# Kernel optimization log

Measured on AMD Instinct MI355X. Metric: run time of the kernel, lower is better.

Reference implementation:

```python
import jax, jax.numpy as jnp
import numpy as np

N_FACTORS = 8
T_BINS = 512
N_NEURONS = 512
N_TRIALS = 128
JITTER = 1e-3


def setup_inputs() -> dict:
    key = jax.random.key(0)
    k1, k2, k3, k4, k5 = jax.random.split(key, 5)
    return {
        "spike_data": jax.random.normal(k1, (N_TRIALS, N_NEURONS, T_BINS), dtype=jnp.float32),
        "Cm": jax.random.normal(k2, (N_NEURONS, N_FACTORS), dtype=jnp.float32),
        "dm": jax.random.normal(k3, (N_NEURONS,), dtype=jnp.float32),
        "r_diag": jax.random.uniform(k4, (N_NEURONS,), dtype=jnp.float32),
        "gamma_m": jax.random.uniform(k5, (N_FACTORS,), dtype=jnp.float32),
    }


def reference(spike_data, Cm, dm, r_diag, gamma_m):
    """GPFA e-step posterior mean.

    Faithful to Multi_populations_GPFA: per-factor SE-kernel GP covariances
    (make_K_big), block-striped inverse (make_K_big_inv), precision
    M = K_big_inv + blockdiag(C' R^-1 C), minv = inv(M) (inv_persymm returns
    exactly inv(M) for persymmetric M), x_mean = minv @ vec(C' R^-1 (y - d)).
    Row ordering is index = t * n_factors + f, matching K_big[i::F, i::F].
    """
    F = N_FACTORS
    n_trials, n_neurons, T = spike_data.shape
    dtype = spike_data.dtype

    # Per-factor GP covariances: K_f = (1-jitter)*exp(-gamma_f/2 * Tdif^2) + jitter*I
    t = jnp.arange(T, dtype=dtype)
    Tdif2 = (t[:, None] - t[None, :]) ** 2                      # (T, T)
    K = (1.0 - JITTER) * jnp.exp(-0.5 * gamma_m[:, None, None] * Tdif2) \
        + JITTER * jnp.eye(T, dtype=dtype)                       # (F, T, T)
    K_inv = jnp.linalg.inv(K)                                    # batched per factor

    # rinv = diag(1/diag(Rm));  c_rinv = C' R^-1;  c_rinv_c = C' R^-1 C
    rinv = 1.0 / r_diag                                          # (N,)
    c_rinv = Cm.T * rinv[None, :]                                # (F, N)
    c_rinv_c = c_rinv @ Cm                                       # (F, F)

    # M[t,i,u,j] = K_inv[i,t,u]*delta_ij + c_rinv_c[i,j]*delta_tu
    eyeF = jnp.eye(F, dtype=dtype)
    eyeT = jnp.eye(T, dtype=dtype)
    M = (jnp.einsum('ftu,ij->tiuj', K_inv, eyeF)
         + jnp.einsum('tu,ij->tiuj', eyeT, c_rinv_c)).reshape(F * T, F * T)
    minv = jnp.linalg.inv(M)                                     # (F*T, F*T)

    # term1[t*F+f, trial] = (C' R^-1 (y - d))[f, trial, t]
    dif = spike_data - dm[None, :, None]                         # (trials, N, T)
    term1 = jnp.einsum('fn,rnt->tfr', c_rinv, dif).reshape(F * T, n_trials)

    x_mean = (minv @ term1).reshape(T, F, n_trials)              # (T, F, trials)
    return jnp.transpose(x_mean, (2, 1, 0))                      # (trials, F, T)
```

## Files before the change

### kernel.cpp

```cpp
#include <hip/hip_runtime.h>


#define NF 8
#define TBINS 512
#define NNEU 512
#define NTRI 128
#define PAD 68

#define OFF_A0     0
#define OFF_A1     2097152
#define OFF_CRVT   4194304
#define OFF_CRVVT  4198400
#define OFF_CCT    4202496
#define OFF_CD     4202560
#define OFF_CDV    4202624
#define OFF_RINV   4202688
#define OFF_LAM    4203200
#define OFF_VF     4203216
#define OFF_BT     4203280
#define OFF_XT     4727568
#define OFF_PP0    5251856
#define OFF_PP1    5284624

__device__ __forceinline__ void load8(float* v, const float* ptr){
  float4 a = ((const float4*)ptr)[0];
  float4 b = ((const float4*)ptr)[1];
  v[0]=a.x; v[1]=a.y; v[2]=a.z; v[3]=a.w;
  v[4]=b.x; v[5]=b.y; v[6]=b.z; v[7]=b.w;
}
__device__ __forceinline__ void store8(float* ptr, const float* v){
  ((float4*)ptr)[0] = make_float4(v[0],v[1],v[2],v[3]);
  ((float4*)ptr)[1] = make_float4(v[4],v[5],v[6],v[7]);
}

__device__ __forceinline__ float rlane(float v, int l){
  return __int_as_float(__builtin_amdgcn_readlane(__float_as_int(v), l));
}

template<int KK>
__device__ __forceinline__ void gj_reg_step(float (&c)[64], int lane){
  float pivot = rlane(c[KK], KK);
  float pinv  = 1.0f / pivot;
  float newr  = c[KK] * pinv;
  bool iskk = (lane == KK);
  #pragma unroll
  for (int i = 0; i < KK; ++i){
    float pc = rlane(c[i], KK);
    c[i] = iskk ? (-pc * pinv) : (c[i] - pc * newr);
  }
  #pragma unroll
  for (int i = KK + 1; i < 64; ++i){
    float pc = rlane(c[i], KK);
    c[i] = iskk ? (-pc * pinv) : (c[i] - pc * newr);
  }
  c[KK] = iskk ? pinv : newr;
}

template<int KK> struct GJChain {
  static __device__ __forceinline__ void run(float (&c)[64], int lane){
    gj_reg_step<KK>(c, lane);
    GJChain<KK + 1>::run(c, lane);
  }
};
template<> struct GJChain<64> {
  static __device__ __forceinline__ void run(float (&c)[64], int lane){}
};

__global__ void prep_kernel(const float* __restrict__ Cm, const float* __restrict__ dm,
                            const float* __restrict__ r_diag,
                            float* __restrict__ crvT, float* __restrict__ ccT,
                            float* __restrict__ cd, float* __restrict__ rinv){
  __shared__ float s_crv[NNEU*NF];
  __shared__ float s_cm[NNEU*NF];
  __shared__ float s_dm[NNEU];
  int tid = threadIdx.x;
  float ri = 1.0f / r_diag[tid];
  rinv[tid] = ri;
  s_dm[tid] = dm[tid];
  #pragma unroll
  for (int f = 0; f < NF; ++f){
    float cv = Cm[tid*NF + f];
    s_cm[tid*NF + f] = cv;
    float v = cv * ri;
    s_crv[tid*NF + f] = v;
    crvT[tid*NF + f] = v;
  }
  __syncthreads();
  if (tid < 64){
    int f = tid >> 3, g = tid & 7;
    float acc = 0.f;
    for (int n = 0; n < NNEU; ++n) acc += s_crv[n*NF+f] * s_cm[n*NF+g];
    ccT[tid] = acc;
  } else if (tid < 72){
    int f = tid - 64;
    float acc = 0.f;
    for (int n = 0; n < NNEU; ++n) acc += s_crv[n*NF+f] * s_dm[n];
    cd[f] = acc;
  }
}

__global__ void eig8_kernel(const float* __restrict__ ccT,
                            float* __restrict__ Vf, float* __restrict__ lam){
  int lane = threadIdx.x & 63;
  int a = lane >> 3, b = lane & 7;
  float Av = ccT[lane];
  float Vv = (a == b) ? 1.0f : 0.0f;
  for (int sw = 0; sw < 8; ++sw){
    for (int p = 0; p < 7; ++p){
      for (int q = p + 1; q < 8; ++q){
        float apq = __shfl(Av, p*8 + q, 64);
        if (fabsf(apq) < 1e-20f) continue;
        float app = __shfl(Av, p*8 + p, 64);
        float aqq = __shfl(Av, q*8 + q, 64);
        float beta = (aqq - app) / (2.0f * apq);
        float tt = ((beta >= 0.0f) ? 1.0f : -1.0f) / (fabsf(beta) + sqrtf(1.0f + beta*beta));
        float c = 1.0f / sqrtf(1.0f + tt*tt);
        float s = tt * c;
        int bp = (b == p) ? q : (b == q) ? p : b;
        float Ac = __shfl(Av, a*8 + bp, 64);
        float Vc = __shfl(Vv, a*8 + bp, 64);
        if (b == p)      { Av = c*Av - s*Ac;  Vv = c*Vv - s*Vc; }
        else if (b == q) { Av = s*Ac + c*Av;  Vv = s*Vc + c*Vv; }
        int ap = (a == p) ? q : (a == q) ? p : a;
        float Ar = __shfl(Av, ap*8 + b, 64);
        if (a == p)      Av = c*Av - s*Ar;
        else if (a == q) Av = s*Ar + c*Av;
      }
    }
  }
  if (a == b) lam[a] = Av;
  Vf[lane] = Vv;
}

__global__ void rotv_kernel(const float* __restrict__ crvT, const float* __restrict__ cd,
                            const float* __restrict__ Vf,
                            float* __restrict__ crvVT, float* __restrict__ cdV){
  __shared__ float Vl[64];
  int tid = threadIdx.x;
  if (tid < 64) Vl[tid] = Vf[tid];
  __syncthreads();
  float cv[8], ov[8];
  load8(cv, crvT + tid*8);
  #pragma unroll
  for (int i = 0; i < 8; ++i){
    float s = 0.f;
    #pragma unroll
    for (int f = 0; f < 8; ++f) s += Vl[f*8+i] * cv[f];
    ov[i] = s;
  }
  store8(crvVT + tid*8, ov);
  if (tid < 8){
    float s = 0.f;
    #pragma unroll
    for (int f = 0; f < 8; ++f) s += Vl[f*8+tid] * cd[f];
    cdV[tid] = s;
  }
}

__global__ void buildK_kernel(const float* __restrict__ gamma, float* __restrict__ A0){
  int f = blockIdx.y;
  int idx = blockIdx.x*256 + threadIdx.x;
  int t = idx >> 9, u = idx & 511;
  float g = gamma[f];
  float d = (float)(t - u);
  float v = 0.999f * expf(-0.5f * g * d * d);
  if (t == u) v += 1.0e-3f;
  A0[(size_t)f*TBINS*TBINS + idx] = v;
}

__global__ void buildG_kernel(const float* __restrict__ A0, const float* __restrict__ lam,
                              float* __restrict__ A1){
  int idx = blockIdx.x*256 + threadIdx.x;
  float s = 0.f;
  #pragma unroll
  for (int f2 = 0; f2 < NF; ++f2) s += A0[(size_t)f2*TBINS*TBINS + idx];
  bool diag = ((idx >> 9) == (idx & 511));
  #pragma unroll
  for (int i = 0; i < NF; ++i)
    A1[(size_t)i*TBINS*TBINS + idx] = s + (diag ? lam[i] : 0.f);
}

__global__ __launch_bounds__(64) void gj_pivot0(const float* __restrict__ A,
                                                float* __restrict__ Pout){
  int f = blockIdx.x;
  int lane = threadIdx.x;
  const float* Af = A + (size_t)f*TBINS*TBINS;
  float c[64];
  #pragma unroll
  for (int i = 0; i < 64; ++i) c[i] = Af[(size_t)i*TBINS + lane];
  GJChain<0>::run(c, lane);
  #pragma unroll
  for (int i = 0; i < 64; ++i) Pout[f*4096 + i*64 + lane] = c[i];
}

#define ACC4(tm, fm) \
  tm[0] += fm.x*s0.x + fm.y*s1.x + fm.z*s2.x + fm.w*s3.x; \
  tm[1] += fm.x*s0.y + fm.y*s1.y + fm.z*s2.y + fm.w*s3.y; \
  tm[2] += fm.x*s0.z + fm.y*s1.z + fm.z*s2.z + fm.w*s3.z; \
  tm[3] += fm.x*s0.w + fm.y*s1.w + fm.z*s2.w + fm.w*s3.w;

__global__ __launch_bounds__(256) void gj_apply(const float* __restrict__ src,
                                                float* __restrict__ dst,
                                                const float* __restrict__ Pin,
                                                float* __restrict__ Pout,
                                                int k, int inv_next){
  __shared__ float P[64*PAD];
  __shared__ float Q[64*PAD];
  __shared__ float F[64*PAD];
  int f  = blockIdx.y;
  int ti = blockIdx.x >> 3, tj = blockIdx.x & 7;
  int tid = threadIdx.x;
  const float* A = src + (size_t)f*TBINS*TBINS;
  float* D = dst + (size_t)f*TBINS*TBINS;

  for (int v = tid; v < 1024; v += 256){
    int r = v >> 4, c4 = (v & 15) << 2;
    *(float4*)&P[r*PAD + c4] = *(const float4*)(Pin + f*4096 + r*64 + c4);
  }
  if (tj != k){
    for (int v = tid; v < 1024; v += 256){
      int r = v >> 4, c4 = (v & 15) << 2;
      *(float4*)&Q[r*PAD + c4] = *(const float4*)(A + (size_t)(k*64+r)*TBINS + tj*64 + c4);
    }
  }
  if (ti != k){
    for (int v = tid; v < 1024; v += 256){
      int r = v >> 4, c4 = (v & 15) << 2;
      *(float4*)&F[r*PAD + c4] = *(const float4*)(A + (size_t)(ti*64+r)*TBINS + k*64 + c4);
    }
  }
  __syncthreads();

  int jg = (tid & 15) << 2;
  int ib = (tid >> 4) << 2;

  if (tj == k){
    if (ti == k){
      for (int v = tid; v < 1024; v += 256){
        int r = v >> 4, c4 = (v & 15) << 2;
        *(float4*)(D + (size_t)(k*64+r)*TBINS + k*64 + c4) = *(float4*)&P[r*PAD + c4];
      }
      return;
    }
    float w[4][4] = {{0.f,0.f,0.f,0.f},{0.f,0.f,0.f,0.f},{0.f,0.f,0.f,0.f},{0.f,0.f,0.f,0.f}};
    for (int u4 = 0; u4 < 64; u4 += 4){
      float4 f0 = *(float4*)&F[(ib+0)*PAD + u4];
      float4 f1 = *(float4*)&F[(ib+1)*PAD + u4];
      float4 f2 = *(float4*)&F[(ib+2)*PAD + u4];
      float4 f3 = *(float4*)&F[(ib+3)*PAD + u4];
      float4 s0 = *(float4*)&P[(u4+0)*PAD + jg];
      float4 s1 = *(float4*)&P[(u4+1)*PAD + jg];
      float4 s2 = *(float4*)&P[(u4+2)*PAD + jg];
      float4 s3 = *(float4*)&P[(u4+3)*PAD + jg];
      ACC4(w[0], f0); ACC4(w[1], f1); ACC4(w[2], f2); ACC4(w[3], f3);
    }
    #pragma unroll
    for (int m = 0; m < 4; ++m)
      *(float4*)(D + (size_t)(ti*64+ib+m)*TBINS + k*64 + jg)
        = make_float4(-w[m][0], -w[m][1], -w[m][2], -w[m][3]);
    return;
  }

  float t[4][4] = {{0.f,0.f,0.f,0.f},{0.f,0.f,0.f,0.f},{0.f,0.f,0.f,0.f},{0.f,0.f,0.f,0.f}};
  for (int u = 0; u < 64; ++u){
    float4 pv = *(float4*)&P[u*PAD + ib];
    float4 qv = *(float4*)&Q[u*PAD + jg];
    t[0][0]+=pv.x*qv.x; t[0][1]+=pv.x*qv.y; t[0][2]+=pv.x*qv.z; t[0][3]+=pv.x*qv.w;
    t[1][0]+=pv.y*qv.x; t[1][1]+=pv.y*qv.y; t[1][2]+=pv.y*qv.z; t[1][3]+=pv.y*qv.w;
    t[2][0]+=pv.z*qv.x; t[2][1]+=pv.z*qv.y; t[2][2]+=pv.z*qv.z; t[2][3]+=pv.z*qv.w;
    t[3][0]+=pv.w*qv.x; t[3][1]+=pv.w*qv.y; t[3][2]+=pv.w*qv.z; t[3][3]+=pv.w*qv.w;
  }
  if (ti == k){
    #pragma unroll
    for (int m = 0; m < 4; ++m)
      *(float4*)(D + (size_t)(k*64+ib+m)*TBINS + tj*64 + jg)
        = make_float4(t[m][0],t[m][1],t[m][2],t[m][3]);
    return;
  }
  __syncthreads();
  #pragma unroll
  for (int m = 0; m < 4; ++m)
    *(float4*)&Q[(ib+m)*PAD + jg] = make_float4(t[m][0],t[m][1],t[m][2],t[m][3]);
  __syncthreads();

  float w[4][4] = {{0.f,0.f,0.f,0.f},{0.f,0.f,0.f,0.f},{0.f,0.f,0.f,0.f},{0.f,0.f,0.f,0.f}};
  for (int u4 = 0; u4 < 64; u4 += 4){
    float4 f0 = *(float4*)&F[(ib+0)*PAD + u4];
    float4 f1 = *(float4*)&F[(ib+1)*PAD + u4];
    float4 f2 = *(float4*)&F[(ib+2)*PAD + u4];
    float4 f3 = *(float4*)&F[(ib+3)*PAD + u4];
    float4 s0 = *(float4*)&Q[(u4+0)*PAD + jg];
    float4 s1 = *(float4*)&Q[(u4+1)*PAD + jg];
    float4 s2 = *(float4*)&Q[(u4+2)*PAD + jg];
    float4 s3 = *(float4*)&Q[(u4+3)*PAD + jg];
    ACC4(w[0], f0); ACC4(w[1], f1); ACC4(w[2], f2); ACC4(w[3], f3);
  }
  #pragma unroll
  for (int m = 0; m < 4; ++m){
    float4 av = *(const float4*)(A + (size_t)(ti*64+ib+m)*TBINS + tj*64 + jg);
    float4 dv = make_float4(av.x - w[m][0], av.y - w[m][1], av.z - w[m][2], av.w - w[m][3]);
    *(float4*)(D + (size_t)(ti*64+ib+m)*TBINS + tj*64 + jg) = dv;
    w[m][0] = dv.x; w[m][1] = dv.y; w[m][2] = dv.z; w[m][3] = dv.w;
  }

  if (inv_next && ti == k+1 && tj == k+1){
    __syncthreads();
    #pragma unroll
    for (int m = 0; m < 4; ++m)
      *(float4*)&P[(ib+m)*PAD + jg] = make_float4(w[m][0],w[m][1],w[m][2],w[m][3]);
    __syncthreads();
    if (tid < 64){
      float c[64];
      #pragma unroll
      for (int i = 0; i < 64; ++i) c[i] = P[i*PAD + tid];
      GJChain<0>::run(c, tid);
      #pragma unroll
      for (int i = 0; i < 64; ++i) Pout[f*4096 + i*64 + tid] = c[i];
    }
  }
}

__global__ void term1_kernel(const float* __restrict__ spike, const float* __restrict__ crvVT,
                             const float* __restrict__ cdV, float* __restrict__ bt){
  __shared__ float crl[NNEU*NF];
  __shared__ float ot[128][17];
  int t0 = blockIdx.x * 16;
  int c0 = blockIdx.y * 16;
  int tid = threadIdx.x;
  int tl = tid & 15, cl = tid >> 4;
  for (int n2 = tid; n2 < NNEU*NF; n2 += 256) crl[n2] = crvVT[n2];
  __syncthreads();
  float acc[8] = {0.f,0.f,0.f,0.f,0.f,0.f,0.f,0.f};
  const float* Sp = spike + (size_t)(c0+cl)*NNEU*TBINS + t0 + tl;
  for (int n = 0; n < NNEU; n += 4){
    float s0 = Sp[(size_t)(n+0)*TBINS];
    float s1 = Sp[(size_t)(n+1)*TBINS];
    float s2 = Sp[(size_t)(n+2)*TBINS];
    float s3 = Sp[(size_t)(n+3)*TBINS];
    #pragma unroll
    for (int i = 0; i < 8; ++i)
      acc[i] += crl[(n+0)*8+i]*s0 + crl[(n+1)*8+i]*s1 + crl[(n+2)*8+i]*s2 + crl[(n+3)*8+i]*s3;
  }
  #pragma unroll
  for (int i = 0; i < 8; ++i) ot[tl*8+i][cl] = acc[i] - cdV[i];
  __syncthreads();
  int row = tid >> 1, off = (tid & 1) * 8;
  int tt = t0 + (row >> 3), ii = row & 7;
  float* dst = bt + (size_t)(tt*8+ii)*NTRI + c0 + off;
  #pragma unroll
  for (int k = 0; k < 8; ++k) dst[k] = ot[row][off+k];
}

__global__ void gemm_kernel(const float* __restrict__ H, const float* __restrict__ bt,
                            float* __restrict__ xt){
  __shared__ float Ht[32][68];
  __shared__ float Bt[64][128];
  int i  = blockIdx.y;
  int t0 = blockIdx.x * 32;
  int tid = threadIdx.x;
  int gt = tid >> 5;
  int gc = tid & 31;
  float acc[4][4] = {{0.f,0.f,0.f,0.f},{0.f,0.f,0.f,0.f},{0.f,0.f,0.f,0.f},{0.f,0.f,0.f,0.f}};
  const float* Hi = H + (size_t)i*TBINS*TBINS;
  for (int uc = 0; uc < 8; ++uc){
    int u0 = uc*64;
    __syncthreads();
    for (int v = tid; v < 512; v += 256){
      int r = v >> 4, c4 = (v & 15) << 2;
      *(float4*)&Ht[r][c4] = *(const float4*)(Hi + (size_t)(t0+r)*TBINS + u0 + c4);
    }
    for (int v = tid; v < 2048; v += 256){
      int r = v >> 5, c4 = (v & 31) << 2;
      *(float4*)&Bt[r][c4] = *(const float4*)(bt + (size_t)((u0+r)*8 + i)*NTRI + c4);
    }
    __syncthreads();
    for (int u = 0; u < 64; ++u){
      float h0 = Ht[gt*4+0][u], h1 = Ht[gt*4+1][u], h2 = Ht[gt*4+2][u], h3 = Ht[gt*4+3][u];
      float b0 = Bt[u][gc], b1 = Bt[u][gc+32], b2 = Bt[u][gc+64], b3 = Bt[u][gc+96];
      acc[0][0] += h0*b0; acc[0][1] += h0*b1; acc[0][2] += h0*b2; acc[0][3] += h0*b3;
      acc[1][0] += h1*b0; acc[1][1] += h1*b1; acc[1][2] += h1*b2; acc[1][3] += h1*b3;
      acc[2][0] += h2*b0; acc[2][1] += h2*b1; acc[2][2] += h2*b2; acc[2][3] += h2*b3;
      acc[3][0] += h3*b0; acc[3][1] += h3*b1; acc[3][2] += h3*b2; acc[3][3] += h3*b3;
    }
  }
  #pragma unroll
  for (int m = 0; m < 4; ++m)
    #pragma unroll
    for (int j = 0; j < 4; ++j)
      xt[(size_t)((t0 + gt*4 + m)*8 + i)*NTRI + gc + 32*j] = acc[m][j];
}

__global__ void output_kernel(const float* __restrict__ xt, const float* __restrict__ Vf,
                              float* __restrict__ out){
  __shared__ float T[128][68];
  __shared__ float Vl[64];
  int t0 = blockIdx.x * 64, c0 = blockIdx.y * 16;
  int tid = threadIdx.x;
  if (tid < 64) Vl[tid] = Vf[tid];
  __syncthreads();
  for (int idx = tid; idx < 1024; idx += 256){
    int tl = idx >> 4, cl = idx & 15;
    float xv[8];
    #pragma unroll
    for (int i = 0; i < 8; ++i)
      xv[i] = xt[(size_t)((t0+tl)*8+i)*NTRI + c0 + cl];
    #pragma unroll
    for (int f = 0; f < 8; ++f){
      float s = 0.f;
      #pragma unroll
      for (int i = 0; i < 8; ++i) s += Vl[f*8+i] * xv[i];
      T[cl*8+f][tl] = s;
    }
  }
  __syncthreads();
  int row = tid >> 1, half = tid & 1;
  int cc = c0 + (row >> 3), ff = row & 7;
  float* dst = out + (size_t)cc*NF*TBINS + ff*TBINS + t0 + half*32;
  #pragma unroll
  for (int k = 0; k < 8; ++k)
    ((float4*)dst)[k] = *(float4*)&T[row][half*32 + k*4];
}

extern "C" void kernel_launch(void* const* d_in, const int* in_sizes, int n_in,
                              void* d_out, int out_size, void* d_ws, size_t ws_size,
                              hipStream_t stream) {
  const float* spike  = (const float*)d_in[0];
  const float* Cm     = (const float*)d_in[1];
  const float* dm     = (const float*)d_in[2];
  const float* r_diag = (const float*)d_in[3];
  const float* gamma  = (const float*)d_in[4];
  float* out = (float*)d_out;
  float* ws = (float*)d_ws;

  float*  A0    = ws + OFF_A0;
  float*  A1    = ws + OFF_A1;
  float*  crvT  = ws + OFF_CRVT;
  float*  crvVT = ws + OFF_CRVVT;
  float*  ccT   = ws + OFF_CCT;
  float*  cd    = ws + OFF_CD;
  float*  cdV   = ws + OFF_CDV;
  float*  rinv  = ws + OFF_RINV;
  float*  lam   = ws + OFF_LAM;
  float*  Vf    = ws + OFF_VF;
  float*  bt    = ws + OFF_BT;
  float*  xt    = ws + OFF_XT;
  float*  Pb[2] = { ws + OFF_PP0, ws + OFF_PP1 };

  prep_kernel<<<1, 512, 0, stream>>>(Cm, dm, r_diag, crvT, ccT, cd, rinv);
  eig8_kernel<<<1, 64, 0, stream>>>(ccT, Vf, lam);
  rotv_kernel<<<1, 512, 0, stream>>>(crvT, cd, Vf, crvVT, cdV);
  buildK_kernel<<<dim3(1024, 8), 256, 0, stream>>>(gamma, A0);

  gj_pivot0<<<8, 64, 0, stream>>>(A0, Pb[0]);
  {
    float* s = A0; float* d = A1;
    for (int k = 0; k < 8; ++k){
      gj_apply<<<dim3(64, 8), 256, 0, stream>>>(s, d, Pb[k&1], Pb[(k+1)&1], k, (k < 7) ? 1 : 0);
      float* tmp = s; s = d; d = tmp;
    }
  }
  buildG_kernel<<<1024, 256, 0, stream>>>(A0, lam, A1);
  gj_pivot0<<<8, 64, 0, stream>>>(A1, Pb[0]);
  {
    float* s = A1; float* d = A0;
    for (int k = 0; k < 8; ++k){
      gj_apply<<<dim3(64, 8), 256, 0, stream>>>(s, d, Pb[k&1], Pb[(k+1)&1], k, (k < 7) ? 1 : 0);
      float* tmp = s; s = d; d = tmp;
    }
  }
  term1_kernel<<<dim3(32, 8), 256, 0, stream>>>(spike, crvVT, cdV, bt);
  gemm_kernel<<<dim3(16, 8), 256, 0, stream>>>(A1, bt, xt);
  output_kernel<<<dim3(8, 8), 256, 0, stream>>>(xt, Vf, out);
}
```

Before: 1.272 ms.

## Split term1 neuron reduction across blocks and add partial-sum reduce kernel

The term1 projection kernel now splits the 512-neuron reduction into four chunks along a third grid dimension, giving four times as many blocks and a smaller shared-memory footprint per block. Partial sums go to scratch space reused from the A0 buffer. A new reduce kernel adds the four partials and subtracts the C'R^-1 d offset. The inner loop also uses float4 shared-memory loads and a deeper unroll. This trades an extra launch and extra global traffic for better occupancy on a kernel that previously launched only 256 blocks.

```diff
diff --git a/kernel.cpp b/kernel.cpp
--- a/kernel.cpp
+++ b/kernel.cpp
@@ -321,34 +321,53 @@
 }
 
 __global__ void term1_kernel(const float* __restrict__ spike, const float* __restrict__ crvVT,
-                             const float* __restrict__ cdV, float* __restrict__ bt){
-  __shared__ float crl[NNEU*NF];
+                             float* __restrict__ btp){
+  __shared__ float crl[128*NF];
   __shared__ float ot[128][17];
   int t0 = blockIdx.x * 16;
   int c0 = blockIdx.y * 16;
+  int n0 = blockIdx.z << 7;
   int tid = threadIdx.x;
   int tl = tid & 15, cl = tid >> 4;
-  for (int n2 = tid; n2 < NNEU*NF; n2 += 256) crl[n2] = crvVT[n2];
+  ((float4*)crl)[tid] = ((const float4*)(crvVT + n0*NF))[tid];
   __syncthreads();
   float acc[8] = {0.f,0.f,0.f,0.f,0.f,0.f,0.f,0.f};
-  const float* Sp = spike + (size_t)(c0+cl)*NNEU*TBINS + t0 + tl;
-  for (int n = 0; n < NNEU; n += 4){
-    float s0 = Sp[(size_t)(n+0)*TBINS];
-    float s1 = Sp[(size_t)(n+1)*TBINS];
-    float s2 = Sp[(size_t)(n+2)*TBINS];
-    float s3 = Sp[(size_t)(n+3)*TBINS];
-    #pragma unroll
-    for (int i = 0; i < 8; ++i)
-      acc[i] += crl[(n+0)*8+i]*s0 + crl[(n+1)*8+i]*s1 + crl[(n+2)*8+i]*s2 + crl[(n+3)*8+i]*s3;
-  }
-  #pragma unroll
-  for (int i = 0; i < 8; ++i) ot[tl*8+i][cl] = acc[i] - cdV[i];
+  const float* Sp = spike + (size_t)(c0+cl)*NNEU*TBINS + (size_t)n0*TBINS + t0 + tl;
+  for (int n = 0; n < 128; n += 8){
+    float s[8];
+    #pragma unroll
+    for (int j = 0; j < 8; ++j) s[j] = Sp[(size_t)(n+j)*TBINS];
+    #pragma unroll
+    for (int j = 0; j < 8; ++j){
+      float4 ca = *(float4*)&crl[(n+j)*8];
+      float4 cb = *(float4*)&crl[(n+j)*8+4];
+      acc[0] += ca.x*s[j]; acc[1] += ca.y*s[j]; acc[2] += ca.z*s[j]; acc[3] += ca.w*s[j];
+      acc[4] += cb.x*s[j]; acc[5] += cb.y*s[j]; acc[6] += cb.z*s[j]; acc[7] += cb.w*s[j];
+    }
+  }
+  #pragma unroll
+  for (int i = 0; i < 8; ++i) ot[tl*8+i][cl] = acc[i];
   __syncthreads();
   int row = tid >> 1, off = (tid & 1) * 8;
   int tt = t0 + (row >> 3), ii = row & 7;
-  float* dst = bt + (size_t)(tt*8+ii)*NTRI + c0 + off;
+  float* dst = btp + (size_t)blockIdx.z*524288 + (size_t)(tt*8+ii)*NTRI + c0 + off;
   #pragma unroll
   for (int k = 0; k < 8; ++k) dst[k] = ot[row][off+k];
+}
+
+__global__ void term1_reduce(const float* __restrict__ btp, const float* __restrict__ cdV,
+                             float* __restrict__ bt){
+  int idx = blockIdx.x*256 + threadIdx.x;
+  const float4* p = (const float4*)btp;
+  float4 a = p[idx];
+  float4 b = p[idx + 131072];
+  float4 c = p[idx + 262144];
+  float4 d = p[idx + 393216];
+  float cv = cdV[(idx >> 5) & 7];
+  ((float4*)bt)[idx] = make_float4(a.x+b.x+c.x+d.x - cv,
+                                   a.y+b.y+c.y+d.y - cv,
+                                   a.z+b.z+c.z+d.z - cv,
+                                   a.w+b.w+c.w+d.w - cv);
 }
 
 __global__ void gemm_kernel(const float* __restrict__ H, const float* __restrict__ bt,
@@ -468,7 +487,8 @@
       float* tmp = s; s = d; d = tmp;
     }
   }
-  term1_kernel<<<dim3(32, 8), 256, 0, stream>>>(spike, crvVT, cdV, bt);
+  term1_kernel<<<dim3(32, 8, 4), 256, 0, stream>>>(spike, crvVT, A0);
+  term1_reduce<<<512, 256, 0, stream>>>(A0, cdV, bt);
   gemm_kernel<<<dim3(16, 8), 256, 0, stream>>>(A1, bt, xt);
   output_kernel<<<dim3(8, 8), 256, 0, stream>>>(xt, Vf, out);
 }
```

After: 1.246 ms. 1.02x faster.
